# Kernel tuning notes

Measured on AMD Instinct MI355X. Metric: run time of the kernel, lower is better.

The kernel has to match this reference:

```python
import jax, jax.numpy as jnp
import numpy as np

ATT_DIM = 768
N_HEADS = 4
N_LABELS = 2000
NEG_INF = -1e6


def setup_inputs() -> dict:
    key = jax.random.key(0)
    k1, k2, k3, k4, k5, k6 = jax.random.split(key, 6)
    B, S, D = 4, 3072, ATT_DIM
    h = jax.random.normal(k1, (B, S, D), dtype=jnp.float32)
    attention_mask = jnp.ones((B, S), dtype=jnp.int32)
    label_feat = jax.random.normal(k2, (N_LABELS * N_HEADS, D), dtype=jnp.float32)
    # nn.Linear W: weight [D, D], bias [D]
    W_w = jax.random.normal(k3, (D, D), dtype=jnp.float32) * 0.02
    W_b = jnp.zeros((D,), dtype=jnp.float32)
    # classifier: weight [num_labels, D], bias [num_labels]
    cls_w = jax.random.normal(k4, (N_LABELS, D), dtype=jnp.float32) * 0.02
    cls_b = jnp.zeros((N_LABELS,), dtype=jnp.float32)
    return {"h": h, "attention_mask": attention_mask, "label_feat": label_feat,
            "W_w": W_w, "W_b": W_b, "cls_w": cls_w, "cls_b": cls_b}


def reference(h, attention_mask, label_feat, W_w, W_b, cls_w, cls_b):
    # h: [B,S,D]; label_feat: [E*H, D]
    B, S, D = h.shape
    E = label_feat.shape[0] // N_HEADS
    z = jnp.tanh(h @ W_w.T + W_b)                       # [B,S,D]
    u = label_feat.reshape(E, N_HEADS, D)               # [E,H,D]
    # score 'abd,ecd->aebc' -> [B,E,S,H]
    score = jnp.einsum('bsd,ehd->besh', z, u)
    mask = attention_mask.astype(bool)[:, None, :, None]  # [B,1,S,1]
    score = jnp.where(mask, score, NEG_INF)
    alpha = jax.nn.softmax(score, axis=2)               # softmax over seq
    # m 'abd,aebc->aedc' -> [B,E,D,H]
    m = jnp.einsum('bsd,besh->bedh', h, alpha)
    m = m.max(axis=-1)                                  # head max-pool -> [B,E,D]
    logits = jnp.sum(cls_w[None] * m, axis=2) + cls_b   # [B,E]
    return logits, m
```

## Files before the change

kernel.cpp:

```cpp
#include <hip/hip_runtime.h>
#include <hip/hip_bf16.h>

typedef _Float16 f16;
typedef _Float16 half8 __attribute__((ext_vector_type(8)));
typedef _Float16 half4v __attribute__((ext_vector_type(4)));
typedef float f32x4 __attribute__((ext_vector_type(4)));
typedef float f32x16 __attribute__((ext_vector_type(16)));

#define B_ 4
#define S_ 3072
#define D_ 768
#define E_ 2000
#define NEG_INF -1.0e6f

#define GLD16(gsrc, ldst)                                                     \
  __builtin_amdgcn_global_load_lds(                                           \
      (const __attribute__((address_space(1))) void*)(gsrc),                  \
      (__attribute__((address_space(3))) void*)(ldst), 16, 0, 0)

__global__ __launch_bounds__(256) void k_transpose(const float* __restrict__ h,
                                                   f16* __restrict__ ht) {
  __shared__ f16 tile[64][65];
  int b = blockIdx.z, s0 = blockIdx.x * 64, d0 = blockIdx.y * 64;
  int t = threadIdx.x, tx = t & 63, ty = t >> 6;
  const float* src = h + ((size_t)b * S_ + s0) * D_ + d0;
#pragma unroll
  for (int i = 0; i < 16; ++i) {
    int sl = i * 4 + ty;
    tile[sl][tx] = (f16)src[(size_t)sl * D_ + tx];
  }
  __syncthreads();
  f16* dst = ht + ((size_t)b * D_ + d0) * S_ + s0;
#pragma unroll
  for (int i = 0; i < 16; ++i) {
    int dl = i * 4 + ty;
    dst[(size_t)dl * S_ + tx] = tile[tx][dl];
  }
}

__global__ __launch_bounds__(256) void k_zgemm(const float* __restrict__ h,
                                               const float* __restrict__ W,
                                               const float* __restrict__ bias,
                                               f16* __restrict__ zb) {
  __shared__ f16 As[64][40];
  __shared__ f16 Bs[64][40];
  int i0 = blockIdx.x * 64, j0 = blockIdx.y * 64;
  int t = threadIdx.x, w = t >> 6, lane = t & 63, g = lane >> 4, li = lane & 15;
  int wi = w >> 1, wj = w & 1;

  f32x4 acc[2][2];
#pragma unroll
  for (int a = 0; a < 2; ++a)
#pragma unroll
    for (int b2 = 0; b2 < 2; ++b2) acc[a][b2] = (f32x4){0.f, 0.f, 0.f, 0.f};

  int srow = t >> 2, scol = (t & 3) * 8;
  const float* pA = h + (size_t)(i0 + srow) * D_ + scol;
  const float* pB = W + (size_t)(j0 + srow) * D_ + scol;

  for (int kc = 0; kc < D_; kc += 32) {
    float4 a0 = *(const float4*)(pA + kc);
    float4 a1 = *(const float4*)(pA + kc + 4);
    float4 b0 = *(const float4*)(pB + kc);
    float4 b1 = *(const float4*)(pB + kc + 4);
    half8 av = {(f16)a0.x, (f16)a0.y, (f16)a0.z, (f16)a0.w,
                (f16)a1.x, (f16)a1.y, (f16)a1.z, (f16)a1.w};
    half8 bv = {(f16)b0.x, (f16)b0.y, (f16)b0.z, (f16)b0.w,
                (f16)b1.x, (f16)b1.y, (f16)b1.z, (f16)b1.w};
    *(half8*)&As[srow][scol] = av;
    *(half8*)&Bs[srow][scol] = bv;
    __syncthreads();
#pragma unroll
    for (int it = 0; it < 2; ++it) {
      half8 af = *(const half8*)&As[wi * 32 + it * 16 + li][g * 8];
#pragma unroll
      for (int jt = 0; jt < 2; ++jt) {
        half8 bf = *(const half8*)&Bs[wj * 32 + jt * 16 + li][g * 8];
        acc[it][jt] =
            __builtin_amdgcn_mfma_f32_16x16x32_f16(af, bf, acc[it][jt], 0, 0, 0);
      }
    }
    __syncthreads();
  }
#pragma unroll
  for (int it = 0; it < 2; ++it) {
#pragma unroll
    for (int jt = 0; jt < 2; ++jt) {
      int jj = j0 + wj * 32 + jt * 16 + li;
      float bsv = bias[jj];
#pragma unroll
      for (int r = 0; r < 4; ++r) {
        int ii = i0 + wi * 32 + it * 16 + g * 4 + r;
        float v = acc[it][jt][r] + bsv;
        zb[(size_t)ii * D_ + jj] = (f16)tanhf(v);
      }
    }
  }
}

__global__ __launch_bounds__(512)
void k_attn(const float* __restrict__ lf,
            const f16* __restrict__ zb,
            const f16* __restrict__ ht,
            const int* __restrict__ amask,
            float* __restrict__ out_m) {
  __shared__ __align__(16) char Lds[70432];
  char* KsB = Lds;
  char* CpB = Lds + 49152;
  char* PtB = Lds + 65536;
  float* FacB = (float*)(Lds + 69632);
  float* LfinB = (float*)(Lds + 69888);
  int* MskI = (int*)(Lds + 70144);
  int* RflW = (int*)(Lds + 70400);

  const int fid = blockIdx.x;
  const int x2 = fid & 7, u = fid >> 3;
  const int b = x2 >> 1;
  const int qtile = (x2 & 1) * 64 + u;
  if (qtile >= 125) return;
  const int q0 = qtile * 64;
  const int e0 = qtile * 16;

  const int t = threadIdx.x, w = t >> 6, l = t & 63;
  const int l31 = l & 31, h = l >> 5, h16 = h * 16;
  const int qh = w & 1, kq = w >> 1;
  const int dh = w;

  half8 qf[12];
  {
    const float* qp = lf + (size_t)(q0 + qh * 32 + l31) * D_ + kq * 192 + h * 8;
#pragma unroll
    for (int kf = 0; kf < 12; ++kf) {
      float4 v0 = *(const float4*)(qp + kf * 16);
      float4 v1 = *(const float4*)(qp + kf * 16 + 4);
      qf[kf] = (half8){(f16)v0.x, (f16)v0.y, (f16)v0.z, (f16)v0.w,
                       (f16)v1.x, (f16)v1.y, (f16)v1.z, (f16)v1.w};
    }
  }

  int klds[6], kgsw[6];
#pragma unroll
  for (int k = 0; k < 6; ++k) {
    int lin = (w * 6 + k) * 1024 + l * 16;
    int row = lin / 1536;
    int xo = lin - row * 1536;
    klds[k] = lin;
    kgsw[k] = row * 1536 + (xo ^ ((row & 7) << 4));
  }

  const int am7 = (l & 7) << 4;
  const int abase = l31 * 1536 + kq * 384;

  const int rswz = ((l31 >> 1) & 3) << 4;
  const int cqoff = l31 * 64;

  const int qh_s = w >> 2, qoct = w & 3;
  const int qrow = qoct * 8 + (l >> 3);
  const int swzr = ((qrow >> 1) & 3) << 4;
  const int roff = qrow * 64 + ((8 * (l & 7)) ^ swzr);
  const int qabs = qh_s * 32 + qrow;

  const char* zbB = (const char*)zb + (size_t)b * S_ * 1536;
  const f16* vbase = ht + ((size_t)b * D_ + dh * 96 + l31) * S_ + h * 8;

#pragma unroll
  for (int k = 0; k < 6; ++k) GLD16(zbB + kgsw[k], KsB + klds[k]);
  if (t < 32) MskI[t] = amask[b * S_ + t];
  asm volatile("s_waitcnt vmcnt(0)" ::: "memory");
  __syncthreads();

  float mreg = -3.0e38f, lreg = 0.0f;
  f32x16 oacc[2][3];
#pragma unroll
  for (int a = 0; a < 2; ++a)
#pragma unroll
    for (int d = 0; d < 3; ++d)
#pragma unroll
      for (int j = 0; j < 16; ++j) oacc[a][d][j] = 0.f;

  half8 Vb[6];

  for (int i = 0; i < 96; ++i) {
    const int s0 = i * 32;
    const int s0n = (i < 95) ? s0 + 32 : 0;

    int mnext = (t < 32) ? amask[b * S_ + s0n + t] : 0;

    if (i > 0) {
      int4 fA = *(const int4*)RflW;
      int4 fB = *(const int4*)(RflW + 4);
      int f0 = fA.x | fA.y | fA.z | fA.w;
      int f1 = fB.x | fB.y | fB.z | fB.w;
      if (f0) {
        f32x4 frv[4];
#pragma unroll
        for (int rr = 0; rr < 4; ++rr)
          frv[rr] = *(const f32x4*)(FacB + rr * 8 + h * 4);
#pragma unroll
        for (int dt = 0; dt < 3; ++dt)
#pragma unroll
          for (int j = 0; j < 16; ++j) oacc[0][dt][j] *= frv[j >> 2][j & 3];
      }
      if (f1) {
        f32x4 frv[4];
#pragma unroll
        for (int rr = 0; rr < 4; ++rr)
          frv[rr] = *(const f32x4*)(FacB + 32 + rr * 8 + h * 4);
#pragma unroll
        for (int dt = 0; dt < 3; ++dt)
#pragma unroll
          for (int j = 0; j < 16; ++j) oacc[1][dt][j] *= frv[j >> 2][j & 3];
      }
      half8 pa[2][2];
#pragma unroll
      for (int q2 = 0; q2 < 2; ++q2)
#pragma unroll
        for (int ss = 0; ss < 2; ++ss)
          pa[q2][ss] = *(const half8*)(PtB + q2 * 2048 + cqoff +
                                       ((ss * 32 + h16) ^ rswz));
      __builtin_amdgcn_s_setprio(1);
#pragma unroll
      for (int dt = 0; dt < 3; ++dt)
#pragma unroll
        for (int ss = 0; ss < 2; ++ss)
#pragma unroll
          for (int q2 = 0; q2 < 2; ++q2)
            oacc[q2][dt] = __builtin_amdgcn_mfma_f32_32x32x16_f16(
                pa[q2][ss], Vb[dt * 2 + ss], oacc[q2][dt], 0, 0, 0);
      __builtin_amdgcn_s_setprio(0);
    }

    {
      const f16* vp = vbase + s0;
#pragma unroll
      for (int dt = 0; dt < 3; ++dt)
#pragma unroll
        for (int ss = 0; ss < 2; ++ss)
          Vb[dt * 2 + ss] = *(const half8*)(vp + (size_t)dt * 32 * S_ + ss * 16);
    }

    f32x16 ca;
#pragma unroll
    for (int j = 0; j < 16; ++j) ca[j] = 0.f;
    __builtin_amdgcn_s_setprio(1);
#pragma unroll
    for (int kf = 0; kf < 12; ++kf) {
      half8 a = *(const half8*)(KsB + abase + ((kf * 32 + h16) ^ am7));
      ca = __builtin_amdgcn_mfma_f32_32x32x16_f16(a, qf[kf], ca, 0, 0, 0);
    }
    __builtin_amdgcn_s_setprio(0);

    {
      char* cp = CpB + w * 2048 + cqoff;
#pragma unroll
      for (int rr = 0; rr < 4; ++rr) {
        half4v pk = {(f16)ca[4 * rr], (f16)ca[4 * rr + 1], (f16)ca[4 * rr + 2],
                     (f16)ca[4 * rr + 3]};
        *(half4v*)(cp + ((rr * 16 + h * 8) ^ rswz)) = pk;
      }
    }
    asm volatile("s_waitcnt lgkmcnt(0)" ::: "memory");
    __builtin_amdgcn_s_barrier();

    {
      const char* src = zbB + (size_t)s0n * 1536;
#pragma unroll
      for (int k = 0; k < 6; ++k) GLD16(src + kgsw[k], KsB + klds[k]);
    }
    {
      float p0 = 0.f, p1 = 0.f, p2 = 0.f, p3 = 0.f;
#pragma unroll
      for (int kk = 0; kk < 4; ++kk) {
        half4v pk = *(const half4v*)(CpB + (kk * 2 + qh_s) * 2048 + roff);
        p0 += (float)pk[0];
        p1 += (float)pk[1];
        p2 += (float)pk[2];
        p3 += (float)pk[3];
      }
      int4 m4 = *(const int4*)(MskI + (i & 1) * 32 + 4 * (l & 7));
      if (!m4.x) p0 = NEG_INF;
      if (!m4.y) p1 = NEG_INF;
      if (!m4.z) p2 = NEG_INF;
      if (!m4.w) p3 = NEG_INF;
      float pmax = fmaxf(fmaxf(p0, p1), fmaxf(p2, p3));
      pmax = fmaxf(pmax, __shfl_xor(pmax, 1));
      pmax = fmaxf(pmax, __shfl_xor(pmax, 2));
      pmax = fmaxf(pmax, __shfl_xor(pmax, 4));
      int need = __any(pmax > mreg + 8.0f);
      float Mn = mreg, fec = 1.0f;
      if (need) {
        Mn = fmaxf(mreg, pmax);
        fec = __expf(mreg - Mn);
        mreg = Mn;
      }
      p0 = __expf(p0 - Mn);
      p1 = __expf(p1 - Mn);
      p2 = __expf(p2 - Mn);
      p3 = __expf(p3 - Mn);
      float ts = p0 + p1 + p2 + p3;
      ts += __shfl_xor(ts, 1);
      ts += __shfl_xor(ts, 2);
      ts += __shfl_xor(ts, 4);
      lreg = lreg * fec + ts;
      if ((l & 7) == 0) FacB[qabs] = fec;
      if (l == 0) RflW[w] = need;
      *(half4v*)(PtB + qh_s * 2048 + roff) =
          (half4v){(f16)p0, (f16)p1, (f16)p2, (f16)p3};
    }
    if (t < 32) MskI[((i + 1) & 1) * 32 + t] = mnext;
    asm volatile("s_waitcnt vmcnt(0) lgkmcnt(0)" ::: "memory");
    __builtin_amdgcn_s_barrier();
  }

  {
    int4 fA = *(const int4*)RflW;
    int4 fB = *(const int4*)(RflW + 4);
    int f0 = fA.x | fA.y | fA.z | fA.w;
    int f1 = fB.x | fB.y | fB.z | fB.w;
    if (f0) {
      f32x4 frv[4];
#pragma unroll
      for (int rr = 0; rr < 4; ++rr)
        frv[rr] = *(const f32x4*)(FacB + rr * 8 + h * 4);
#pragma unroll
      for (int dt = 0; dt < 3; ++dt)
#pragma unroll
        for (int j = 0; j < 16; ++j) oacc[0][dt][j] *= frv[j >> 2][j & 3];
    }
    if (f1) {
      f32x4 frv[4];
#pragma unroll
      for (int rr = 0; rr < 4; ++rr)
        frv[rr] = *(const f32x4*)(FacB + 32 + rr * 8 + h * 4);
#pragma unroll
      for (int dt = 0; dt < 3; ++dt)
#pragma unroll
        for (int j = 0; j < 16; ++j) oacc[1][dt][j] *= frv[j >> 2][j & 3];
    }
    half8 pa[2][2];
#pragma unroll
    for (int q2 = 0; q2 < 2; ++q2)
#pragma unroll
      for (int ss = 0; ss < 2; ++ss)
        pa[q2][ss] = *(const half8*)(PtB + q2 * 2048 + cqoff +
                                     ((ss * 32 + h16) ^ rswz));
#pragma unroll
    for (int dt = 0; dt < 3; ++dt)
#pragma unroll
      for (int ss = 0; ss < 2; ++ss)
#pragma unroll
        for (int q2 = 0; q2 < 2; ++q2)
          oacc[q2][dt] = __builtin_amdgcn_mfma_f32_32x32x16_f16(
              pa[q2][ss], Vb[dt * 2 + ss], oacc[q2][dt], 0, 0, 0);
  }

  if ((l & 7) == 0) LfinB[qabs] = lreg;
  __syncthreads();

  f32x4 rlv[2][4];
#pragma unroll
  for (int q2 = 0; q2 < 2; ++q2)
#pragma unroll
    for (int rr = 0; rr < 4; ++rr) {
      f32x4 lv = *(const f32x4*)(LfinB + q2 * 32 + rr * 8 + h * 4);
      rlv[q2][rr] =
          (f32x4){1.0f / lv[0], 1.0f / lv[1], 1.0f / lv[2], 1.0f / lv[3]};
    }
#pragma unroll
  for (int q2 = 0; q2 < 2; ++q2)
#pragma unroll
    for (int dt = 0; dt < 3; ++dt)
#pragma unroll
      for (int rr = 0; rr < 4; ++rr) {
        float mv = oacc[q2][dt][4 * rr + 0] * rlv[q2][rr][0];
        mv = fmaxf(mv, oacc[q2][dt][4 * rr + 1] * rlv[q2][rr][1]);
        mv = fmaxf(mv, oacc[q2][dt][4 * rr + 2] * rlv[q2][rr][2]);
        mv = fmaxf(mv, oacc[q2][dt][4 * rr + 3] * rlv[q2][rr][3]);
        int e_loc = q2 * 8 + rr * 2 + h;
        out_m[((size_t)b * E_ + e0 + e_loc) * D_ + dh * 96 + dt * 32 + l31] = mv;
      }
}

__global__ __launch_bounds__(256) void k_logits(const float* __restrict__ cw,
                                                const float* __restrict__ cb,
                                                const float* __restrict__ m,
                                                float* __restrict__ out) {
  int t = threadIdx.x, w = t >> 6, lane = t & 63;
  int rid = blockIdx.x * 4 + w;
  int b = rid / E_, e = rid - b * E_;
  const float* mr = m + (size_t)rid * D_;
  const float* cr = cw + (size_t)e * D_;
  float acc = 0.f;
#pragma unroll
  for (int i = 0; i < 12; ++i) acc += cr[i * 64 + lane] * mr[i * 64 + lane];
#pragma unroll
  for (int off = 32; off >= 1; off >>= 1) acc += __shfl_xor(acc, off);
  if (lane == 0) out[rid] = acc + cb[e];
}

extern "C" void kernel_launch(void* const* d_in, const int* in_sizes, int n_in,
                              void* d_out, int out_size, void* d_ws, size_t ws_size,
                              hipStream_t stream) {
  const float* h = (const float*)d_in[0];
  const int* amask = (const int*)d_in[1];
  const float* lf = (const float*)d_in[2];
  const float* Ww = (const float*)d_in[3];
  const float* Wb = (const float*)d_in[4];
  const float* cw = (const float*)d_in[5];
  const float* cb = (const float*)d_in[6];
  float* out = (float*)d_out;

  f16* zb = (f16*)d_ws;
  f16* ht = (f16*)((char*)d_ws + 18874368);

  k_transpose<<<dim3(48, 12, 4), 256, 0, stream>>>(h, ht);
  k_zgemm<<<dim3(192, 12), 256, 0, stream>>>(h, Ww, Wb, zb);
  k_attn<<<512, 512, 0, stream>>>(lf, zb, ht, amask, out + 8000);
  k_logits<<<2000, 256, 0, stream>>>(cw, cb, out + 8000, out);
}
```

Measured before the change: 628.9 us.

## Shrink attention block to 32 queries with 4 waves, drop software pipelining of PV

The attention kernel is reorganized from 512-thread blocks handling 64 query rows to 256-thread blocks handling 32 rows, launched as 1000 blocks with two blocks per CU. The grid becomes an exact fit, so the idle tail blocks of the old 125-tile mapping go away. LDS use drops enough to allow two resident blocks. The previous overlap, where the PV MFMA of the prior step ran under the next score step, is replaced by an in-iteration PV pass with direct V loads and an extra barrier. Each block now reloads the full K tile per step for only 32 queries, which doubles K traffic per query, and the exposed V load latency plus the extra barrier may cost time.

Result: slower. 892.7 us (+41.9%).

```diff
diff --git a/kernel.cpp b/kernel.cpp
--- a/kernel.cpp
+++ b/kernel.cpp
@@ -98,37 +98,34 @@
   }
 }
 
-__global__ __launch_bounds__(512)
+__global__ __launch_bounds__(256, 2)
 void k_attn(const float* __restrict__ lf,
             const f16* __restrict__ zb,
             const f16* __restrict__ ht,
             const int* __restrict__ amask,
             float* __restrict__ out_m) {
-  __shared__ __align__(16) char Lds[70432];
+  __shared__ __align__(16) char Lds[59920];
   char* KsB = Lds;
   char* CpB = Lds + 49152;
-  char* PtB = Lds + 65536;
-  float* FacB = (float*)(Lds + 69632);
-  float* LfinB = (float*)(Lds + 69888);
-  int* MskI = (int*)(Lds + 70144);
-  int* RflW = (int*)(Lds + 70400);
+  char* PtB = Lds + 57344;
+  float* FacB = (float*)(Lds + 59392);
+  float* LfinB = (float*)(Lds + 59520);
+  int* MskI = (int*)(Lds + 59648);
+  int* RflW = (int*)(Lds + 59904);
 
   const int fid = blockIdx.x;
   const int x2 = fid & 7, u = fid >> 3;
   const int b = x2 >> 1;
-  const int qtile = (x2 & 1) * 64 + u;
-  if (qtile >= 125) return;
-  const int q0 = qtile * 64;
-  const int e0 = qtile * 16;
+  const int qtile = (x2 & 1) * 125 + u;
+  const int q0 = qtile * 32;
+  const int e0 = qtile * 8;
 
   const int t = threadIdx.x, w = t >> 6, l = t & 63;
   const int l31 = l & 31, h = l >> 5, h16 = h * 16;
-  const int qh = w & 1, kq = w >> 1;
-  const int dh = w;
 
   half8 qf[12];
   {
-    const float* qp = lf + (size_t)(q0 + qh * 32 + l31) * D_ + kq * 192 + h * 8;
+    const float* qp = lf + (size_t)(q0 + l31) * D_ + w * 192 + h * 8;
 #pragma unroll
     for (int kf = 0; kf < 12; ++kf) {
       float4 v0 = *(const float4*)(qp + kf * 16);
@@ -138,10 +135,10 @@
     }
   }
 
-  int klds[6], kgsw[6];
-#pragma unroll
-  for (int k = 0; k < 6; ++k) {
-    int lin = (w * 6 + k) * 1024 + l * 16;
+  int klds[12], kgsw[12];
+#pragma unroll
+  for (int k = 0; k < 12; ++k) {
+    int lin = (w * 12 + k) * 1024 + l * 16;
     int row = lin / 1536;
     int xo = lin - row * 1536;
     klds[k] = lin;
@@ -149,95 +146,36 @@
   }
 
   const int am7 = (l & 7) << 4;
-  const int abase = l31 * 1536 + kq * 384;
+  const int abase = l31 * 1536 + w * 384;
 
   const int rswz = ((l31 >> 1) & 3) << 4;
   const int cqoff = l31 * 64;
 
-  const int qh_s = w >> 2, qoct = w & 3;
-  const int qrow = qoct * 8 + (l >> 3);
+  const int qrow = w * 8 + (l >> 3);
   const int swzr = ((qrow >> 1) & 3) << 4;
   const int roff = qrow * 64 + ((8 * (l & 7)) ^ swzr);
-  const int qabs = qh_s * 32 + qrow;
 
   const char* zbB = (const char*)zb + (size_t)b * S_ * 1536;
-  const f16* vbase = ht + ((size_t)b * D_ + dh * 96 + l31) * S_ + h * 8;
-
-#pragma unroll
-  for (int k = 0; k < 6; ++k) GLD16(zbB + kgsw[k], KsB + klds[k]);
+  const f16* vbase = ht + ((size_t)b * D_ + w * 192 + l31) * S_ + h * 8;
+
+#pragma unroll
+  for (int k = 0; k < 12; ++k) GLD16(zbB + kgsw[k], KsB + klds[k]);
   if (t < 32) MskI[t] = amask[b * S_ + t];
   asm volatile("s_waitcnt vmcnt(0)" ::: "memory");
   __syncthreads();
 
   float mreg = -3.0e38f, lreg = 0.0f;
-  f32x16 oacc[2][3];
-#pragma unroll
-  for (int a = 0; a < 2; ++a)
-#pragma unroll
-    for (int d = 0; d < 3; ++d)
-#pragma unroll
-      for (int j = 0; j < 16; ++j) oacc[a][d][j] = 0.f;
-
-  half8 Vb[6];
+  f32x16 oacc[6];
+#pragma unroll
+  for (int d = 0; d < 6; ++d)
+#pragma unroll
+    for (int j = 0; j < 16; ++j) oacc[d][j] = 0.f;
 
   for (int i = 0; i < 96; ++i) {
     const int s0 = i * 32;
     const int s0n = (i < 95) ? s0 + 32 : 0;
 
     int mnext = (t < 32) ? amask[b * S_ + s0n + t] : 0;
-
-    if (i > 0) {
-      int4 fA = *(const int4*)RflW;
-      int4 fB = *(const int4*)(RflW + 4);
-      int f0 = fA.x | fA.y | fA.z | fA.w;
-      int f1 = fB.x | fB.y | fB.z | fB.w;
-      if (f0) {
-        f32x4 frv[4];
-#pragma unroll
-        for (int rr = 0; rr < 4; ++rr)
-          frv[rr] = *(const f32x4*)(FacB + rr * 8 + h * 4);
-#pragma unroll
-        for (int dt = 0; dt < 3; ++dt)
-#pragma unroll
-          for (int j = 0; j < 16; ++j) oacc[0][dt][j] *= frv[j >> 2][j & 3];
-      }
-      if (f1) {
-        f32x4 frv[4];
-#pragma unroll
-        for (int rr = 0; rr < 4; ++rr)
-          frv[rr] = *(const f32x4*)(FacB + 32 + rr * 8 + h * 4);
-#pragma unroll
-        for (int dt = 0; dt < 3; ++dt)
-#pragma unroll
-          for (int j = 0; j < 16; ++j) oacc[1][dt][j] *= frv[j >> 2][j & 3];
-      }
-      half8 pa[2][2];
-#pragma unroll
-      for (int q2 = 0; q2 < 2; ++q2)
-#pragma unroll
-        for (int ss = 0; ss < 2; ++ss)
-          pa[q2][ss] = *(const half8*)(PtB + q2 * 2048 + cqoff +
-                                       ((ss * 32 + h16) ^ rswz));
-      __builtin_amdgcn_s_setprio(1);
-#pragma unroll
-      for (int dt = 0; dt < 3; ++dt)
-#pragma unroll
-        for (int ss = 0; ss < 2; ++ss)
-#pragma unroll
-          for (int q2 = 0; q2 < 2; ++q2)
-            oacc[q2][dt] = __builtin_amdgcn_mfma_f32_32x32x16_f16(
-                pa[q2][ss], Vb[dt * 2 + ss], oacc[q2][dt], 0, 0, 0);
-      __builtin_amdgcn_s_setprio(0);
-    }
-
-    {
-      const f16* vp = vbase + s0;
-#pragma unroll
-      for (int dt = 0; dt < 3; ++dt)
-#pragma unroll
-        for (int ss = 0; ss < 2; ++ss)
-          Vb[dt * 2 + ss] = *(const half8*)(vp + (size_t)dt * 32 * S_ + ss * 16);
-    }
 
     f32x16 ca;
 #pragma unroll
@@ -265,13 +203,13 @@
     {
       const char* src = zbB + (size_t)s0n * 1536;
 #pragma unroll
-      for (int k = 0; k < 6; ++k) GLD16(src + kgsw[k], KsB + klds[k]);
+      for (int k = 0; k < 12; ++k) GLD16(src + kgsw[k], KsB + klds[k]);
     }
     {
       float p0 = 0.f, p1 = 0.f, p2 = 0.f, p3 = 0.f;
 #pragma unroll
       for (int kk = 0; kk < 4; ++kk) {
-        half4v pk = *(const half4v*)(CpB + (kk * 2 + qh_s) * 2048 + roff);
+        half4v pk = *(const half4v*)(CpB + kk * 2048 + roff);
         p0 += (float)pk[0];
         p1 += (float)pk[1];
         p2 += (float)pk[2];
@@ -302,83 +240,66 @@
       ts += __shfl_xor(ts, 2);
       ts += __shfl_xor(ts, 4);
       lreg = lreg * fec + ts;
-      if ((l & 7) == 0) FacB[qabs] = fec;
+      if ((l & 7) == 0) FacB[qrow] = fec;
       if (l == 0) RflW[w] = need;
-      *(half4v*)(PtB + qh_s * 2048 + roff) =
-          (half4v){(f16)p0, (f16)p1, (f16)p2, (f16)p3};
+      *(half4v*)(PtB + roff) = (half4v){(f16)p0, (f16)p1, (f16)p2, (f16)p3};
     }
     if (t < 32) MskI[((i + 1) & 1) * 32 + t] = mnext;
-    asm volatile("s_waitcnt vmcnt(0) lgkmcnt(0)" ::: "memory");
+    asm volatile("s_waitcnt lgkmcnt(0)" ::: "memory");
     __builtin_amdgcn_s_barrier();
-  }
-
-  {
-    int4 fA = *(const int4*)RflW;
-    int4 fB = *(const int4*)(RflW + 4);
-    int f0 = fA.x | fA.y | fA.z | fA.w;
-    int f1 = fB.x | fB.y | fB.z | fB.w;
-    if (f0) {
-      f32x4 frv[4];
-#pragma unroll
-      for (int rr = 0; rr < 4; ++rr)
-        frv[rr] = *(const f32x4*)(FacB + rr * 8 + h * 4);
-#pragma unroll
-      for (int dt = 0; dt < 3; ++dt)
-#pragma unroll
-        for (int j = 0; j < 16; ++j) oacc[0][dt][j] *= frv[j >> 2][j & 3];
-    }
-    if (f1) {
-      f32x4 frv[4];
-#pragma unroll
-      for (int rr = 0; rr < 4; ++rr)
-        frv[rr] = *(const f32x4*)(FacB + 32 + rr * 8 + h * 4);
-#pragma unroll
-      for (int dt = 0; dt < 3; ++dt)
-#pragma unroll
-        for (int j = 0; j < 16; ++j) oacc[1][dt][j] *= frv[j >> 2][j & 3];
-    }
-    half8 pa[2][2];
-#pragma unroll
-    for (int q2 = 0; q2 < 2; ++q2)
-#pragma unroll
-      for (int ss = 0; ss < 2; ++ss)
-        pa[q2][ss] = *(const half8*)(PtB + q2 * 2048 + cqoff +
-                                     ((ss * 32 + h16) ^ rswz));
-#pragma unroll
-    for (int dt = 0; dt < 3; ++dt)
-#pragma unroll
-      for (int ss = 0; ss < 2; ++ss)
-#pragma unroll
-        for (int q2 = 0; q2 < 2; ++q2)
-          oacc[q2][dt] = __builtin_amdgcn_mfma_f32_32x32x16_f16(
-              pa[q2][ss], Vb[dt * 2 + ss], oacc[q2][dt], 0, 0, 0);
-  }
-
-  if ((l & 7) == 0) LfinB[qabs] = lreg;
+
+    {
+      int4 fA = *(const int4*)RflW;
+      int f0 = fA.x | fA.y | fA.z | fA.w;
+      if (f0) {
+        f32x4 frv[4];
+#pragma unroll
+        for (int rr = 0; rr < 4; ++rr)
+          frv[rr] = *(const f32x4*)(FacB + rr * 8 + h * 4);
+#pragma unroll
+        for (int dt = 0; dt < 6; ++dt)
+#pragma unroll
+          for (int j = 0; j < 16; ++j) oacc[dt][j] *= frv[j >> 2][j & 3];
+      }
+      half8 pa0 = *(const half8*)(PtB + cqoff + (h16 ^ rswz));
+      half8 pa1 = *(const half8*)(PtB + cqoff + ((32 + h16) ^ rswz));
+      const f16* vp = vbase + s0;
+      __builtin_amdgcn_s_setprio(1);
+#pragma unroll
+      for (int dt = 0; dt < 6; ++dt) {
+        half8 v0 = *(const half8*)(vp + (size_t)dt * 32 * S_);
+        half8 v1 = *(const half8*)(vp + (size_t)dt * 32 * S_ + 16);
+        oacc[dt] =
+            __builtin_amdgcn_mfma_f32_32x32x16_f16(pa0, v0, oacc[dt], 0, 0, 0);
+        oacc[dt] =
+            __builtin_amdgcn_mfma_f32_32x32x16_f16(pa1, v1, oacc[dt], 0, 0, 0);
+      }
+      __builtin_amdgcn_s_setprio(0);
+    }
+    asm volatile("s_waitcnt vmcnt(0)" ::: "memory");
+    __builtin_amdgcn_s_barrier();
+  }
+
+  if ((l & 7) == 0) LfinB[qrow] = lreg;
   __syncthreads();
 
-  f32x4 rlv[2][4];
-#pragma unroll
-  for (int q2 = 0; q2 < 2; ++q2)
+  f32x4 rlv[4];
+#pragma unroll
+  for (int rr = 0; rr < 4; ++rr) {
+    f32x4 lv = *(const f32x4*)(LfinB + rr * 8 + h * 4);
+    rlv[rr] = (f32x4){1.0f / lv[0], 1.0f / lv[1], 1.0f / lv[2], 1.0f / lv[3]};
+  }
+#pragma unroll
+  for (int dt = 0; dt < 6; ++dt)
 #pragma unroll
     for (int rr = 0; rr < 4; ++rr) {
-      f32x4 lv = *(const f32x4*)(LfinB + q2 * 32 + rr * 8 + h * 4);
-      rlv[q2][rr] =
-          (f32x4){1.0f / lv[0], 1.0f / lv[1], 1.0f / lv[2], 1.0f / lv[3]};
-    }
-#pragma unroll
-  for (int q2 = 0; q2 < 2; ++q2)
-#pragma unroll
-    for (int dt = 0; dt < 3; ++dt)
-#pragma unroll
-      for (int rr = 0; rr < 4; ++rr) {
-        float mv = oacc[q2][dt][4 * rr + 0] * rlv[q2][rr][0];
-        mv = fmaxf(mv, oacc[q2][dt][4 * rr + 1] * rlv[q2][rr][1]);
-        mv = fmaxf(mv, oacc[q2][dt][4 * rr + 2] * rlv[q2][rr][2]);
-        mv = fmaxf(mv, oacc[q2][dt][4 * rr + 3] * rlv[q2][rr][3]);
-        int e_loc = q2 * 8 + rr * 2 + h;
-        out_m[((size_t)b * E_ + e0 + e_loc) * D_ + dh * 96 + dt * 32 + l31] = mv;
-      }
+      float mv = oacc[dt][4 * rr + 0] * rlv[rr][0];
+      mv = fmaxf(mv, oacc[dt][4 * rr + 1] * rlv[rr][1]);
+      mv = fmaxf(mv, oacc[dt][4 * rr + 2] * rlv[rr][2]);
+      mv = fmaxf(mv, oacc[dt][4 * rr + 3] * rlv[rr][3]);
+      int e_loc = rr * 2 + h;
+      out_m[((size_t)b * E_ + e0 + e_loc) * D_ + w * 192 + dt * 32 + l31] = mv;
+    }
 }
 
 __global__ __launch_bounds__(256) void k_logits(const float* __restrict__ cw,
@@ -415,6 +336,6 @@
 
   k_transpose<<<dim3(48, 12, 4), 256, 0, stream>>>(h, ht);
   k_zgemm<<<dim3(192, 12), 256, 0, stream>>>(h, Ww, Wb, zb);
-  k_attn<<<512, 512, 0, stream>>>(lf, zb, ht, amask, out + 8000);
+  k_attn<<<1000, 256, 0, stream>>>(lf, zb, ht, amask, out + 8000);
   k_logits<<<2000, 256, 0, stream>>>(cw, cb, out + 8000, out);
 }
```
